# Optimization experiments

Measured on AMD Instinct MI355X. Metric: run time of the kernel, lower is better.

The kernel has to match this reference:

```python
import jax, jax.numpy as jnp
import numpy as np

DIM = 384
NH = 6
HD = DIM // NH  # 64
WS = (6, 12)    # window_size (dilated_size=[1,1] so total_window_size == window_size)
SS = (3, 6)     # shift_size
N = WS[0] * WS[1]  # 72 tokens per window


def _make_mask(H, W):
    # Faithful replication of SD_attn.create_mask (static, so computed in numpy).
    wh, ww = WS
    sh, sw = SS
    img = np.zeros((H, W), np.float32)
    cnt = 0
    for hs in (slice(0, -wh), slice(-wh, -sh), slice(-sh, None)):
        for wsl in (slice(0, -ww), slice(-ww, 0), slice(0, None)):
            img[hs, wsl] = cnt
            cnt += 1
    # window partition -> (nW, N)
    m = img.reshape(H // wh, wh, W // ww, ww).transpose(0, 2, 1, 3).reshape(-1, wh * ww)
    d = m[:, None, :] - m[:, :, None]  # (nW, N, N), [i,j] = m[j]-m[i]
    return np.where(d != 0, -np.inf, 0.0).astype(np.float32)


def _rope2d(x):
    # 2D axial rotary embedding over the (wh, ww) window grid.
    # x: (M, wh, ww, hd); first half of pair-channels rotated by h-position, second half by w-position.
    wh, ww, hd = x.shape[1], x.shape[2], x.shape[3]
    half = hd // 2
    inv = 1.0 / (10000.0 ** (np.arange(0, half, 2, dtype=np.float32) / half))  # (half//2,)
    ah = np.arange(wh, dtype=np.float32)[:, None] * inv  # (wh, half//2)
    aw = np.arange(ww, dtype=np.float32)[:, None] * inv  # (ww, half//2)
    ang = np.concatenate([
        np.broadcast_to(ah[:, None, :], (wh, ww, half // 2)),
        np.broadcast_to(aw[None, :, :], (wh, ww, half // 2)),
    ], -1)  # (wh, ww, half)
    cos = jnp.asarray(np.cos(ang), dtype=x.dtype)
    sin = jnp.asarray(np.sin(ang), dtype=x.dtype)
    x1, x2 = x[..., 0::2], x[..., 1::2]
    return jnp.stack([x1 * cos - x2 * sin, x1 * sin + x2 * cos], -1).reshape(x.shape)


def setup_inputs() -> dict:
    key = jax.random.key(0)
    ks = jax.random.split(key, 5)
    x = jax.random.normal(ks[0], (2, 192, 384, DIM), jnp.float32)
    w_qkv = 0.02 * jax.random.normal(ks[1], (3 * DIM, DIM), jnp.float32)
    b_qkv = 0.02 * jax.random.normal(ks[2], (3 * DIM,), jnp.float32)
    w_proj = 0.02 * jax.random.normal(ks[3], (DIM, DIM), jnp.float32)
    b_proj = 0.02 * jax.random.normal(ks[4], (DIM,), jnp.float32)
    return {"x": x, "w_qkv": w_qkv, "b_qkv": b_qkv, "w_proj": w_proj, "b_proj": b_proj}


def reference(x, w_qkv, b_qkv, w_proj, b_proj):
    B, H, W, C = x.shape
    wh, ww = WS
    sh, sw = SS
    nH, nWc = H // wh, W // ww
    nwin = nH * nWc
    B_ = B * nwin
    scale = HD ** -0.5

    # cyclic shift + window partition (dilated_size=[1,1] => plain swin windows)
    xs = jnp.roll(x, (-sh, -sw), axis=(1, 2))
    xw = xs.reshape(B, nH, wh, nWc, ww, C).transpose(0, 1, 3, 2, 4, 5).reshape(B_, N, C)

    qkv = (xw @ w_qkv.T + b_qkv).reshape(B_, N, 3, NH, HD).transpose(2, 0, 3, 1, 4)
    q, k, v = qkv[0], qkv[1], qkv[2]  # (B_, NH, N, HD)

    q = _rope2d(q.reshape(-1, wh, ww, HD)).reshape(B_, NH, N, HD)
    k = _rope2d(k.reshape(-1, wh, ww, HD)).reshape(B_, NH, N, HD)

    attn = jnp.einsum('bhnd,bhmd->bhnm', q * scale, k)  # (B_, NH, N, N)
    mask = jnp.asarray(_make_mask(H, W))                 # (nwin, N, N)
    attn = (attn.reshape(B, nwin, NH, N, N) + mask[None, :, None]).reshape(B_, NH, N, N)
    attn = jax.nn.softmax(attn, axis=-1)
    save_attn = attn.mean(axis=1)  # mean over heads -> (B_, N, N)

    out = jnp.einsum('bhnm,bhmd->bhnd', attn, v).transpose(0, 2, 1, 3).reshape(B_, N, C)
    out = out.reshape(B, nH, nWc, wh, ww, C).transpose(0, 1, 3, 2, 4, 5).reshape(B, H, W, C)
    out = jnp.roll(out, (sh, sw), axis=(1, 2))
    out = out @ w_proj.T + b_proj
    return out, save_attn
```

## Files before the change

kernel.cpp:

```cpp
#include <hip/hip_runtime.h>

typedef __attribute__((ext_vector_type(8))) __bf16 bf16x8;
typedef __attribute__((ext_vector_type(4))) float f32x4;
typedef unsigned short u16;
typedef unsigned int u32;

__device__ __forceinline__ u16 f2bf(float x){
  u32 u = __float_as_uint(x);
  return (u16)((u + 0x7fffu + ((u >> 16) & 1u)) >> 16);
}
__device__ __forceinline__ u32 pkbf(float lo, float hi){
  u32 r; asm("v_cvt_pk_bf16_f32 %0, %1, %2" : "=v"(r) : "v"(lo), "v"(hi)); return r;
}

union FragU { uint4 u4; bf16x8 bf; };

__device__ __forceinline__ bf16x8 lds_frag(const unsigned char* smem, int off, int row, int strideB, int kElem){
  int byte = (row * strideB + kElem * 2) ^ ((row & 7) << 4);
  FragU f; f.u4 = *reinterpret_cast<const uint4*>(smem + off + byte);
  return f.bf;
}

typedef __attribute__((address_space(3))) unsigned char lds_u8;
typedef __attribute__((address_space(1))) const unsigned char g_u8;
__device__ __forceinline__ void glds16(const void* g, void* l){
  __builtin_amdgcn_global_load_lds((g_u8*)g, (lds_u8*)l, 16, 0, 0);
}

__global__ void prep_weights(const float* __restrict__ wq, const float* __restrict__ wp,
                             u16* __restrict__ wqb, u16* __restrict__ wpb){
  int i = blockIdx.x * 256 + threadIdx.x;
  wqb[i] = f2bf(wq[i]);
  if (i < 147456) wpb[i] = f2bf(wp[i]);
}

__global__ void prep_x(const float* __restrict__ x, u16* __restrict__ xb){
  size_t i = ((size_t)blockIdx.x * 256 + threadIdx.x) * 8;
  float4 f0 = *reinterpret_cast<const float4*>(x + i);
  float4 f1 = *reinterpret_cast<const float4*>(x + i + 4);
  uint4 q;
  q.x = pkbf(f0.x, f0.y); q.y = pkbf(f0.z, f0.w);
  q.z = pkbf(f1.x, f1.y); q.w = pkbf(f1.z, f1.w);
  *reinterpret_cast<uint4*>(xb + i) = q;
}

#define QA_OFF 0
#define QB_OFF 16384
#define QTC    65536
#define QTS    66688
template<int XB>
__launch_bounds__(512, 2)
__global__ void qkv_gemm_t(const float* __restrict__ x, const u16* __restrict__ xb,
                           const u16* __restrict__ wqb,
                           const float* __restrict__ bq, float* __restrict__ out,
                           u16* __restrict__ vws)
{
  __shared__ __align__(16) unsigned char smem[67840];
  const int tid  = threadIdx.x;
  const int wave = tid >> 6;
  const int lane = tid & 63;
  const int l15  = lane & 15;
  const int lhi  = lane >> 4;
  const int wr   = wave >> 2;
  const int wc   = wave & 3;
  const int bx   = blockIdx.x;
  const int sec  = blockIdx.y;
  const size_t row0 = (size_t)bx * 128;
  const int a    = bx / 3;
  const int bcol = bx - 3 * a;
  const int bIm  = a / 192;
  const int hh   = a % 192;
  const int rh   = (hh >= 3) ? hh - 3 : hh + 189;
  const int wi   = rh / 6;
  const int r6   = rh - wi * 6;
  const int bwin = bIm * 1024 + wi * 32;

  float* tabc = reinterpret_cast<float*>(smem + QTC);
  float* tabs = reinterpret_cast<float*>(smem + QTS);
  if (tid < 288){
    int pos = tid >> 4, m = tid & 15;
    float pv = (pos < 6) ? (float)pos : (float)(pos - 6);
    float ang = pv * __expf(-(float)m * 0.5756462732485114f);
    tabc[tid] = cosf(ang);
    tabs[tid] = sinf(ang);
  }

  f32x4 acc[4][6];
  #pragma unroll
  for (int mt = 0; mt < 4; ++mt)
    #pragma unroll
    for (int nt = 0; nt < 6; ++nt) acc[mt][nt] = 0.0f;

  for (int kk = 0; kk < 6; ++kk){
    if constexpr (XB){
      #pragma unroll
      for (int it = 0; it < 2; ++it){
        int c = it * 512 + tid;
        int rrow = c >> 3, p = c & 7;
        int s = p ^ (rrow & 7);
        glds16(xb + (row0 + rrow) * 384 + kk * 64 + s * 8,
               smem + QA_OFF + c * 16);
      }
    } else {
      int row = tid >> 2;
      int c0  = (tid & 3) << 4;
      const float* src = x + (row0 + row) * 384 + kk * 64 + c0;
      float4 a0 = *reinterpret_cast<const float4*>(src);
      float4 a1 = *reinterpret_cast<const float4*>(src + 4);
      float4 a2 = *reinterpret_cast<const float4*>(src + 8);
      float4 a3 = *reinterpret_cast<const float4*>(src + 12);
      uint4 q0, q1;
      q0.x = pkbf(a0.x, a0.y); q0.y = pkbf(a0.z, a0.w);
      q0.z = pkbf(a1.x, a1.y); q0.w = pkbf(a1.z, a1.w);
      q1.x = pkbf(a2.x, a2.y); q1.y = pkbf(a2.z, a2.w);
      q1.z = pkbf(a3.x, a3.y); q1.w = pkbf(a3.z, a3.w);
      int b0 = (row * 128 + c0 * 2)      ^ ((row & 7) << 4);
      int b1 = (row * 128 + c0 * 2 + 16) ^ ((row & 7) << 4);
      *reinterpret_cast<uint4*>(smem + QA_OFF + b0) = q0;
      *reinterpret_cast<uint4*>(smem + QA_OFF + b1) = q1;
    }
    #pragma unroll
    for (int it = 0; it < 6; ++it){
      int c = it * 512 + tid;
      int n = c >> 3, p = c & 7;
      int s = p ^ (n & 7);
      glds16(wqb + (size_t)(sec * 384 + n) * 384 + kk * 64 + s * 8,
             smem + QB_OFF + c * 16);
    }
    __syncthreads();
    #pragma unroll
    for (int ks = 0; ks < 2; ++ks){
      const int kEl = ks * 32 + lhi * 8;
      bf16x8 af[4], bf[6];
      #pragma unroll
      for (int mt = 0; mt < 4; ++mt)
        af[mt] = lds_frag(smem, QA_OFF, wr * 64 + mt * 16 + l15, 128, kEl);
      #pragma unroll
      for (int nt = 0; nt < 6; ++nt)
        bf[nt] = lds_frag(smem, QB_OFF, wc * 96 + nt * 16 + l15, 128, kEl);
      #pragma unroll
      for (int mt = 0; mt < 4; ++mt)
        #pragma unroll
        for (int nt = 0; nt < 6; ++nt)
          acc[mt][nt] = __builtin_amdgcn_mfma_f32_16x16x32_bf16(af[mt], bf[nt], acc[mt][nt], 0, 0, 0);
    }
    __syncthreads();
  }

  if (sec < 2){
    u16* o16 = (u16*)out;
    #pragma unroll
    for (int nt = 0; nt < 6; ++nt){
      const int ch = wc * 96 + nt * 16 + l15;
      const float bias = bq[sec * 384 + ch];
      const int chh = ch & 63;
      const int p   = chh >> 1;
      const int m   = p & 15;
      const bool isR = (p < 16);
      const bool ev  = ((ch & 1) == 0);
      #pragma unroll
      for (int mt = 0; mt < 4; ++mt){
        #pragma unroll
        for (int r = 0; r < 4; ++r){
          const int i = wr * 64 + mt * 16 + lhi * 4 + r;
          float v = acc[mt][nt][r] + bias;
          float o = __shfl_xor(v, 1);
          int pos = isR ? r6 : (6 + (bcol * 128 + i + 6) % 12);
          float cc = tabc[pos * 16 + m], ssn = tabs[pos * 16 + m];
          float nv = ev ? (v * cc - o * ssn) : (o * ssn + v * cc);
          if (sec == 0) nv *= 0.125f;
          o16[(row0 + i) * 768 + sec * 384 + ch] = f2bf(nv);
        }
      }
    }
  } else {
    #pragma unroll
    for (int mt = 0; mt < 4; ++mt){
      const int ww2 = bcol * 128 + wr * 64 + mt * 16 + lhi * 4;
      const int rw  = (ww2 >= 6) ? ww2 - 6 : ww2 + 378;
      const int wj  = rw / 12;
      const int c0  = rw - wj * 12;
      const int tokb = r6 * 12;
      #pragma unroll
      for (int nt = 0; nt < 6; ++nt){
        const int ch  = wc * 96 + nt * 16 + l15;
        const int h   = ch >> 6;
        const int chh = ch & 63;
        const float bv = bq[768 + ch];
        u32 lo = pkbf(acc[mt][nt][0] + bv, acc[mt][nt][1] + bv);
        u32 hi = pkbf(acc[mt][nt][2] + bv, acc[mt][nt][3] + bv);
        u16* basep = vws + ((size_t)(bwin + wj) * 6 + h) * 5120 + chh * 80;
        if (c0 != 10){
          *reinterpret_cast<u32*>(basep + tokb + c0)     = lo;
          *reinterpret_cast<u32*>(basep + tokb + c0 + 2) = hi;
        } else {
          *reinterpret_cast<u32*>(basep + tokb + 10) = lo;
          const int wj1 = (wj == 31) ? 0 : wj + 1;
          *reinterpret_cast<u32*>(vws + ((size_t)(bwin + wj1) * 6 + h) * 5120 + chh * 80 + tokb) = hi;
        }
      }
    }
  }
}

#define QH4 0
#define KH4 10240
#define VT4 20480
#define SMEM4 30720
__launch_bounds__(320, 5)
__global__ void win_attn4(const u16* __restrict__ vws,
                          float* __restrict__ out)
{
  __shared__ __align__(16) unsigned char smem[SMEM4];
  const int tid  = threadIdx.x;
  const int wave = tid >> 6;
  const int lane = tid & 63;
  const int l15  = lane & 15;
  const int lhi  = lane >> 4;

  const int bid  = blockIdx.x;
  const int wgid = (bid & 7) * 256 + (bid >> 3);
  const int bIdx = wgid >> 10;
  const int win  = wgid & 1023;
  const int wi   = win >> 5;
  const int wj   = win & 31;
  const bool maskWin = (wi == 31);

  auto rowof = [&](int t)->size_t {
    int r = t / 12, c = t - r * 12;
    int hh = wi * 6 + r + 3;  if (hh >= 192) hh -= 192;
    int ww = wj * 12 + c + 6; if (ww >= 384) ww -= 384;
    return ((size_t)bIdx * 192 + hh) * 384 + ww;
  };
  const int qtok = wave * 16 + l15;
  const bool tv = (qtok < 72);
  const size_t qrow = rowof(tv ? qtok : 71);

  const u16* o16c = (const u16*)out;
  u16* ao16 = (u16*)out;
  const u16* vsl = vws + (size_t)win * 30720 + (size_t)bIdx * 31457280;

  float sv[5][4];
  #pragma unroll
  for (int a2 = 0; a2 < 5; ++a2)
    #pragma unroll
    for (int b2 = 0; b2 < 4; ++b2) sv[a2][b2] = 0.0f;

  for (int h = 0; h < 6; ++h){
    #pragma unroll
    for (int it = 0; it < 2; ++it){
      int c = it * 320 + tid;
      int t = c >> 3, p = c & 7;
      size_t row = rowof(t < 72 ? t : 71);
      int s = (p ^ (t & 7)) << 3;
      glds16(o16c + row * 768 + h * 64 + s,       smem + QH4 + c * 16);
      glds16(o16c + row * 768 + 384 + h * 64 + s, smem + KH4 + c * 16);
      glds16(vsl + (size_t)h * 5120 + c * 8,      smem + VT4 + c * 16);
    }
    __syncthreads();

    f32x4 pf[5];
    #pragma unroll
    for (int nt = 0; nt < 5; ++nt) pf[nt] = 0.0f;
    __builtin_amdgcn_s_setprio(1);
    #pragma unroll
    for (int ks = 0; ks < 2; ++ks){
      const int kEl = ks * 32 + lhi * 8;
      bf16x8 qf = lds_frag(smem, QH4, qtok, 128, kEl);
      #pragma unroll
      for (int nt = 0; nt < 5; ++nt){
        bf16x8 kf = lds_frag(smem, KH4, nt * 16 + l15, 128, kEl);
        pf[nt] = __builtin_amdgcn_mfma_f32_16x16x32_bf16(kf, qf, pf[nt], 0, 0, 0);
      }
    }
    __builtin_amdgcn_s_setprio(0);

    float mx = -1e30f;
    #pragma unroll
    for (int nt = 0; nt < 5; ++nt)
      #pragma unroll
      for (int r = 0; r < 4; ++r){
        const int kk2 = nt * 16 + lhi * 4 + r;
        bool valid = (kk2 < 72) && (!maskWin || ((kk2 < 36) == (qtok < 36)));
        float val = valid ? pf[nt][r] : -1e30f;
        pf[nt][r] = val;
        mx = fmaxf(mx, val);
      }
    mx = fmaxf(mx, __shfl_xor(mx, 16));
    mx = fmaxf(mx, __shfl_xor(mx, 32));
    float sm = 0.0f;
    #pragma unroll
    for (int nt = 0; nt < 5; ++nt)
      #pragma unroll
      for (int r = 0; r < 4; ++r){
        float e = __expf(pf[nt][r] - mx);
        pf[nt][r] = e; sm += e;
      }
    sm += __shfl_xor(sm, 16);
    sm += __shfl_xor(sm, 32);
    const float inv = 1.0f / sm;
    u32 pp[5][2];
    #pragma unroll
    for (int nt = 0; nt < 5; ++nt){
      float p0 = pf[nt][0] * inv, p1 = pf[nt][1] * inv;
      float p2 = pf[nt][2] * inv, p3 = pf[nt][3] * inv;
      sv[nt][0] += p0; sv[nt][1] += p1; sv[nt][2] += p2; sv[nt][3] += p3;
      pp[nt][0] = pkbf(p0, p1);
      pp[nt][1] = pkbf(p2, p3);
    }

    f32x4 oacc[4];
    #pragma unroll
    for (int nt = 0; nt < 4; ++nt) oacc[nt] = 0.0f;
    #pragma unroll
    for (int ks = 0; ks < 3; ++ks){
      FragU pb;
      u32 w[4];
      #pragma unroll
      for (int w_ = 0; w_ < 4; ++w_){
        int srcLane = l15 + 16 * ((lane >> 4 & 1) * 2 + (w_ >> 1));
        u32 c0 = __shfl(pp[ks * 2][w_ & 1], srcLane);
        u32 c1 = (ks * 2 + 1 < 5) ? __shfl(pp[ks * 2 + 1][w_ & 1], srcLane) : 0u;
        w[w_] = (lhi & 2) ? c1 : c0;
      }
      pb.u4.x = w[0]; pb.u4.y = w[1]; pb.u4.z = w[2]; pb.u4.w = w[3];
      const int kEl = ks * 32 + lhi * 8;
      __builtin_amdgcn_s_setprio(1);
      #pragma unroll
      for (int nt = 0; nt < 4; ++nt){
        FragU vf;
        vf.u4 = *reinterpret_cast<const uint4*>(smem + VT4 + (nt * 16 + l15) * 160 + kEl * 2);
        oacc[nt] = __builtin_amdgcn_mfma_f32_16x16x32_bf16(vf.bf, pb.bf, oacc[nt], 0, 0, 0);
      }
      __builtin_amdgcn_s_setprio(0);
    }
    if (tv){
      u16* ao = ao16 + qrow * 768 + h * 64;
      #pragma unroll
      for (int nt = 0; nt < 4; ++nt){
        uint2 pk;
        pk.x = pkbf(oacc[nt][0], oacc[nt][1]);
        pk.y = pkbf(oacc[nt][2], oacc[nt][3]);
        *reinterpret_cast<uint2*>(ao + nt * 16 + lhi * 4) = pk;
      }
    }
    __syncthreads();
  }

  if (tv){
    float* so = out + 56623104ull + (size_t)wgid * 5184 + (size_t)qtok * 72;
    const float c6 = 1.0f / 6.0f;
    #pragma unroll
    for (int nt = 0; nt < 4; ++nt){
      float4 v4; v4.x = sv[nt][0]*c6; v4.y = sv[nt][1]*c6; v4.z = sv[nt][2]*c6; v4.w = sv[nt][3]*c6;
      *reinterpret_cast<float4*>(so + nt * 16 + lhi * 4) = v4;
    }
    if (lhi < 2){
      float4 v4; v4.x = sv[4][0]*c6; v4.y = sv[4][1]*c6; v4.z = sv[4][2]*c6; v4.w = sv[4][3]*c6;
      *reinterpret_cast<float4*>(so + 64 + lhi * 4) = v4;
    }
  }
}

#define VT3 0
#define P3  16384
__launch_bounds__(320, 4)
__global__ void win_attn_fb(const float* __restrict__ x,
                            const u16* __restrict__ wqb,
                            const float* __restrict__ bq,
                            float* __restrict__ out)
{
  __shared__ __align__(16) unsigned char smem[36864];
  const int tid  = threadIdx.x;
  const int wave = tid >> 6;
  const int lane = tid & 63;
  const int l15  = lane & 15;
  const int lhi  = lane >> 4;

  const int wgid = blockIdx.x;
  const int bIdx = wgid >> 10;
  const int win  = wgid & 1023;
  const int wi   = win >> 5;
  const int wj   = win & 31;
  const bool maskWin = (wi == 31);

  auto rowof = [&](int t)->int {
    int r = t / 12, c = t - r * 12;
    int hh = wi * 6 + r + 3;  if (hh >= 192) hh -= 192;
    int ww = wj * 12 + c + 6; if (ww >= 384) ww -= 384;
    return (bIdx * 192 + hh) * 384 + ww;
  };
  const int qtok = wave * 16 + l15;
  const int qrow = rowof(qtok < 72 ? qtok : 71);
  int krow[5];
  #pragma unroll
  for (int nt = 0; nt < 5; ++nt) krow[nt] = rowof(nt * 16 + l15 < 72 ? nt * 16 + l15 : 71);
  const bool tv = (qtok < 72);

  bf16x8 xfrag[12];
  {
    const float* xp = x + (size_t)qrow * 384;
    #pragma unroll
    for (int ks = 0; ks < 12; ++ks){
      uint4 q; q.x = 0; q.y = 0; q.z = 0; q.w = 0;
      if (tv){
        float4 f0 = *reinterpret_cast<const float4*>(xp + ks * 32 + lhi * 8);
        float4 f1 = *reinterpret_cast<const float4*>(xp + ks * 32 + lhi * 8 + 4);
        q.x = pkbf(f0.x, f0.y); q.y = pkbf(f0.z, f0.w);
        q.z = pkbf(f1.x, f1.y); q.w = pkbf(f1.z, f1.w);
      }
      FragU f; f.u4 = q; xfrag[ks] = f.bf;
    }
  }

  const u16* o16 = (const u16*)out;
  u16* ao16 = (u16*)out;
  const u16* wv = wqb + 768 * 384;

  float sv[5][4];
  #pragma unroll
  for (int a2 = 0; a2 < 5; ++a2)
    #pragma unroll
    for (int b2 = 0; b2 < 4; ++b2) sv[a2][b2] = 0.0f;

  for (int h = 0; h < 6; ++h){
    {
      f32x4 vacc[4];
      #pragma unroll
      for (int nt = 0; nt < 4; ++nt) vacc[nt] = 0.0f;
      #pragma unroll
      for (int ks = 0; ks < 12; ++ks){
        const int kEl = ks * 32 + lhi * 8;
        #pragma unroll
        for (int nt = 0; nt < 4; ++nt){
          FragU f;
          f.u4 = *reinterpret_cast<const uint4*>(wv + (size_t)(h * 64 + nt * 16 + l15) * 384 + kEl);
          vacc[nt] = __builtin_amdgcn_mfma_f32_16x16x32_bf16(xfrag[ks], f.bf, vacc[nt], 0, 0, 0);
        }
      }
      #pragma unroll
      for (int nt = 0; nt < 4; ++nt){
        const int chl = nt * 16 + l15;
        const float bv = bq[768 + h * 64 + chl];
        const int t0 = wave * 16 + lhi * 4;
        uint2 pk;
        pk.x = pkbf(vacc[nt][0] + bv, vacc[nt][1] + bv);
        pk.y = pkbf(vacc[nt][2] + bv, vacc[nt][3] + bv);
        int byte = (chl * 256 + t0 * 2) ^ ((chl & 7) << 4);
        *reinterpret_cast<uint2*>(smem + VT3 + byte) = pk;
      }
    }

    f32x4 pf[5];
    #pragma unroll
    for (int nt = 0; nt < 5; ++nt) pf[nt] = 0.0f;
    #pragma unroll
    for (int ks = 0; ks < 2; ++ks){
      const int kEl = ks * 32 + lhi * 8;
      FragU qf;
      qf.u4 = *reinterpret_cast<const uint4*>(o16 + (size_t)qrow * 768 + h * 64 + kEl);
      #pragma unroll
      for (int nt = 0; nt < 5; ++nt){
        FragU kf;
        kf.u4 = *reinterpret_cast<const uint4*>(o16 + (size_t)krow[nt] * 768 + 384 + h * 64 + kEl);
        pf[nt] = __builtin_amdgcn_mfma_f32_16x16x32_bf16(kf.bf, qf.bf, pf[nt], 0, 0, 0);
      }
    }

    float mx = -1e30f;
    #pragma unroll
    for (int nt = 0; nt < 5; ++nt)
      #pragma unroll
      for (int r = 0; r < 4; ++r){
        const int kk2 = nt * 16 + lhi * 4 + r;
        bool valid = (kk2 < 72) && (!maskWin || ((kk2 < 36) == (qtok < 36)));
        float val = valid ? pf[nt][r] : -1e30f;
        pf[nt][r] = val;
        mx = fmaxf(mx, val);
      }
    mx = fmaxf(mx, __shfl_xor(mx, 16));
    mx = fmaxf(mx, __shfl_xor(mx, 32));
    float sm = 0.0f;
    #pragma unroll
    for (int nt = 0; nt < 5; ++nt)
      #pragma unroll
      for (int r = 0; r < 4; ++r){
        float e = __expf(pf[nt][r] - mx);
        pf[nt][r] = e; sm += e;
      }
    sm += __shfl_xor(sm, 16);
    sm += __shfl_xor(sm, 32);
    const float inv = 1.0f / sm;
    #pragma unroll
    for (int nt = 0; nt < 5; ++nt)
      #pragma unroll
      for (int r = 0; r < 4; ++r){
        float pv2 = pf[nt][r] * inv;
        pf[nt][r] = pv2;
        sv[nt][r] += pv2;
      }

    #pragma unroll
    for (int nt = 0; nt < 5; ++nt){
      const int k0 = nt * 16 + lhi * 4;
      uint2 pk;
      pk.x = pkbf(pf[nt][0], pf[nt][1]);
      pk.y = pkbf(pf[nt][2], pf[nt][3]);
      int byte = (qtok * 256 + k0 * 2) ^ ((qtok & 7) << 4);
      *reinterpret_cast<uint2*>(smem + P3 + byte) = pk;
    }
    {
      int byte = (qtok * 256 + (80 + lhi * 4) * 2) ^ ((qtok & 7) << 4);
      uint2 z; z.x = 0; z.y = 0;
      *reinterpret_cast<uint2*>(smem + P3 + byte) = z;
    }
    __syncthreads();

    f32x4 oacc[4];
    #pragma unroll
    for (int nt = 0; nt < 4; ++nt) oacc[nt] = 0.0f;
    #pragma unroll
    for (int ks = 0; ks < 3; ++ks){
      const int kEl = ks * 32 + lhi * 8;
      bf16x8 pfr = lds_frag(smem, P3, qtok, 256, kEl);
      #pragma unroll
      for (int nt = 0; nt < 4; ++nt){
        bf16x8 vf = lds_frag(smem, VT3, nt * 16 + l15, 256, kEl);
        oacc[nt] = __builtin_amdgcn_mfma_f32_16x16x32_bf16(vf, pfr, oacc[nt], 0, 0, 0);
      }
    }
    if (tv){
      u16* ao = ao16 + (size_t)qrow * 768 + h * 64;
      #pragma unroll
      for (int nt = 0; nt < 4; ++nt){
        uint2 pk;
        pk.x = pkbf(oacc[nt][0], oacc[nt][1]);
        pk.y = pkbf(oacc[nt][2], oacc[nt][3]);
        *reinterpret_cast<uint2*>(ao + nt * 16 + lhi * 4) = pk;
      }
    }
    __syncthreads();
  }

  if (tv){
    float* so = out + 56623104ull + (size_t)wgid * 5184 + (size_t)qtok * 72;
    const float c6 = 1.0f / 6.0f;
    #pragma unroll
    for (int nt = 0; nt < 4; ++nt){
      float4 v4; v4.x = sv[nt][0]*c6; v4.y = sv[nt][1]*c6; v4.z = sv[nt][2]*c6; v4.w = sv[nt][3]*c6;
      *reinterpret_cast<float4*>(so + nt * 16 + lhi * 4) = v4;
    }
    if (lhi < 2){
      float4 v4; v4.x = sv[4][0]*c6; v4.y = sv[4][1]*c6; v4.z = sv[4][2]*c6; v4.w = sv[4][3]*c6;
      *reinterpret_cast<float4*>(so + 64 + lhi * 4) = v4;
    }
  }
}

#define A2_OFF 0
#define B2_OFF 16384
#define SMEM2  65536
__launch_bounds__(512, 2)
__global__ void proj_gemm(const u16* __restrict__ wpb, const float* __restrict__ bp,
                          float* __restrict__ out)
{
  __shared__ __align__(16) unsigned char smem[SMEM2];
  unsigned char* base = smem;

  const int tid  = threadIdx.x;
  const int wave = tid >> 6;
  const int lane = tid & 63;
  const int l15  = lane & 15;
  const int lhi  = lane >> 4;
  const int wr   = wave >> 2;
  const int wc   = wave & 3;
  const size_t row0 = (size_t)blockIdx.x * 128;
  const u16* aog = (const u16*)out;

  f32x4 acc[4][6];
  #pragma unroll
  for (int mt = 0; mt < 4; ++mt)
    #pragma unroll
    for (int nt = 0; nt < 6; ++nt) acc[mt][nt] = 0.0f;

  for (int kk = 0; kk < 6; ++kk){
    #pragma unroll
    for (int it = 0; it < 2; ++it){
      int c = it * 512 + wave * 64 + lane;
      int rrow = c >> 3, p = c & 7;
      int s = p ^ (rrow & 7);
      glds16(aog + (row0 + rrow) * 768 + kk * 64 + s * 8,
             base + A2_OFF + (it * 512 + wave * 64) * 16);
    }
    #pragma unroll
    for (int it = 0; it < 6; ++it){
      int c = it * 512 + wave * 64 + lane;
      int n = c >> 3, p = c & 7;
      int s = p ^ (n & 7);
      glds16(wpb + (size_t)n * 384 + kk * 64 + s * 8,
             base + B2_OFF + (it * 512 + wave * 64) * 16);
    }
    __syncthreads();
    #pragma unroll
    for (int ks = 0; ks < 2; ++ks){
      const int kEl = ks * 32 + lhi * 8;
      bf16x8 af[4], bf[6];
      #pragma unroll
      for (int mt = 0; mt < 4; ++mt)
        af[mt] = lds_frag(base, A2_OFF, wr * 64 + mt * 16 + l15, 128, kEl);
      #pragma unroll
      for (int nt = 0; nt < 6; ++nt)
        bf[nt] = lds_frag(base, B2_OFF, wc * 96 + nt * 16 + l15, 128, kEl);
      #pragma unroll
      for (int mt = 0; mt < 4; ++mt)
        #pragma unroll
        for (int nt = 0; nt < 6; ++nt)
          acc[mt][nt] = __builtin_amdgcn_mfma_f32_16x16x32_bf16(af[mt], bf[nt], acc[mt][nt], 0, 0, 0);
    }
    __syncthreads();
  }

  float bpv[6];
  #pragma unroll
  for (int nt = 0; nt < 6; ++nt) bpv[nt] = bp[wc * 96 + nt * 16 + l15];
  #pragma unroll
  for (int mt = 0; mt < 4; ++mt)
    #pragma unroll
    for (int nt = 0; nt < 6; ++nt){
      const int ch = wc * 96 + nt * 16 + l15;
      #pragma unroll
      for (int r = 0; r < 4; ++r){
        size_t grow = row0 + wr * 64 + mt * 16 + lhi * 4 + r;
        out[grow * 384 + ch] = acc[mt][nt][r] + bpv[nt];
      }
    }
}

extern "C" void kernel_launch(void* const* d_in, const int* in_sizes, int n_in,
                              void* d_out, int out_size, void* d_ws, size_t ws_size,
                              hipStream_t stream)
{
  const float* x  = (const float*)d_in[0];
  const float* wq = (const float*)d_in[1];
  const float* bq = (const float*)d_in[2];
  const float* wp = (const float*)d_in[3];
  const float* bp = (const float*)d_in[4];
  float* out = (float*)d_out;

  u16* wqb = (u16*)d_ws;
  u16* wpb = (u16*)((char*)d_ws + 442368 * 2);
  u16* vws = (u16*)((char*)d_ws + 1179648);
  u16* xb  = (u16*)((char*)d_ws + 127008768);

  const bool big  = ws_size >= 127008768ull;
  const bool big2 = ws_size >= 240254976ull;

  prep_weights<<<1728, 256, 0, stream>>>(wq, wp, wqb, wpb);
  if (big2){
    prep_x<<<27648, 256, 0, stream>>>(x, xb);
    qkv_gemm_t<1><<<dim3(1152, 3), 512, 0, stream>>>(x, xb, wqb, bq, out, vws);
    win_attn4<<<2048, 320, 0, stream>>>(vws, out);
  } else if (big){
    qkv_gemm_t<0><<<dim3(1152, 3), 512, 0, stream>>>(x, nullptr, wqb, bq, out, vws);
    win_attn4<<<2048, 320, 0, stream>>>(vws, out);
  } else {
    qkv_gemm_t<0><<<dim3(1152, 2), 512, 0, stream>>>(x, nullptr, wqb, bq, out, vws);
    win_attn_fb<<<2048, 320, 0, stream>>>(x, wqb, bq, out);
  }
  proj_gemm<<<1152, 512, 0, stream>>>(wpb, bp, out);
}
```

Before: 710.9 us.

## Add smaller-tile double-buffered QKV and projection GEMMs with direct-register A loads

```diff
diff --git a/kernel.cpp b/kernel.cpp
--- a/kernel.cpp
+++ b/kernel.cpp
@@ -44,13 +44,162 @@
   *reinterpret_cast<uint4*>(xb + i) = q;
 }
 
+#define B6STR 12288
+#define T6C   24576
+#define T6S   25728
+__launch_bounds__(512, 4)
+__global__ void qkv_gemm2(const u16* __restrict__ xb, const u16* __restrict__ wqb,
+                          const float* __restrict__ bq, float* __restrict__ out,
+                          u16* __restrict__ vws)
+{
+  __shared__ __align__(16) unsigned char smem[26880];
+  const int tid  = threadIdx.x;
+  const int wave = tid >> 6;
+  const int lane = tid & 63;
+  const int l15  = lane & 15;
+  const int lhi  = lane >> 4;
+  const int wr   = wave >> 2;
+  const int wc   = wave & 3;
+  const int bx   = blockIdx.x;
+  const int ny   = blockIdx.y;
+  const int sec  = blockIdx.z;
+  const size_t row0 = (size_t)bx * 128;
+  const int a    = bx / 3;
+  const int bcol = bx - 3 * a;
+  const int bIm  = a / 192;
+  const int hh   = a % 192;
+  const int rh   = (hh >= 3) ? hh - 3 : hh + 189;
+  const int wi   = rh / 6;
+  const int r6   = rh - wi * 6;
+  const int bwin = bIm * 1024 + wi * 32;
+
+  float* tabc = reinterpret_cast<float*>(smem + T6C);
+  float* tabs = reinterpret_cast<float*>(smem + T6S);
+  if (tid < 288){
+    int pos = tid >> 4, m = tid & 15;
+    float pv = (pos < 6) ? (float)pos : (float)(pos - 6);
+    float ang = pv * __expf(-(float)m * 0.5756462732485114f);
+    tabc[tid] = cosf(ang);
+    tabs[tid] = sinf(ang);
+  }
+
+  const u16* bsec = wqb + (size_t)(sec * 384 + ny * 192) * 384;
+  auto stageB = [&](int t, int bufOff){
+    {
+      int c = tid, row = c >> 2, ccd = c & 3;
+      int ccs = ccd ^ ((row >> 1) & 3);
+      glds16(bsec + (size_t)row * 384 + t * 32 + ccs * 8, smem + bufOff + c * 16);
+    }
+    if (tid < 256){
+      int c = 512 + tid, row = c >> 2, ccd = c & 3;
+      int ccs = ccd ^ ((row >> 1) & 3);
+      glds16(bsec + (size_t)row * 384 + t * 32 + ccs * 8, smem + bufOff + c * 16);
+    }
+  };
+
+  const u16* abase = xb + (row0 + wr * 64 + l15) * 384 + lhi * 8;
+
+  f32x4 acc[4][3];
+  #pragma unroll
+  for (int mt = 0; mt < 4; ++mt)
+    #pragma unroll
+    for (int nt = 0; nt < 3; ++nt) acc[mt][nt] = 0.0f;
+
+  FragU a_cur[4], a_nxt[4];
+  #pragma unroll
+  for (int mt = 0; mt < 4; ++mt)
+    a_cur[mt].u4 = *reinterpret_cast<const uint4*>(abase + mt * 6144);
+  stageB(0, 0);
+  __syncthreads();
+
+  int buf = 0;
+  for (int t = 0; t < 12; ++t){
+    if (t < 11){
+      stageB(t + 1, buf ^ B6STR);
+      #pragma unroll
+      for (int mt = 0; mt < 4; ++mt)
+        a_nxt[mt].u4 = *reinterpret_cast<const uint4*>(abase + mt * 6144 + (t + 1) * 32);
+    }
+    FragU bf[3];
+    #pragma unroll
+    for (int nt = 0; nt < 3; ++nt){
+      int rown = wc * 48 + nt * 16 + l15;
+      int byte = buf + rown * 64 + ((lhi ^ ((rown >> 1) & 3)) << 4);
+      bf[nt].u4 = *reinterpret_cast<const uint4*>(smem + byte);
+    }
+    #pragma unroll
+    for (int mt = 0; mt < 4; ++mt)
+      #pragma unroll
+      for (int nt = 0; nt < 3; ++nt)
+        acc[mt][nt] = __builtin_amdgcn_mfma_f32_16x16x32_bf16(a_cur[mt].bf, bf[nt].bf, acc[mt][nt], 0, 0, 0);
+    __syncthreads();
+    #pragma unroll
+    for (int mt = 0; mt < 4; ++mt) a_cur[mt] = a_nxt[mt];
+    buf ^= B6STR;
+  }
+
+  if (sec < 2){
+    u16* o16 = (u16*)out;
+    #pragma unroll
+    for (int nt = 0; nt < 3; ++nt){
+      const int ch = ny * 192 + wc * 48 + nt * 16 + l15;
+      const float bias = bq[sec * 384 + ch];
+      const int chh = ch & 63;
+      const int p   = chh >> 1;
+      const int m   = p & 15;
+      const bool isR = (p < 16);
+      const bool ev  = ((ch & 1) == 0);
+      #pragma unroll
+      for (int mt = 0; mt < 4; ++mt){
+        #pragma unroll
+        for (int r = 0; r < 4; ++r){
+          const int i = wr * 64 + mt * 16 + lhi * 4 + r;
+          float v = acc[mt][nt][r] + bias;
+          float o = __shfl_xor(v, 1);
+          int pos = isR ? r6 : (6 + (bcol * 128 + i + 6) % 12);
+          float cc = tabc[pos * 16 + m], ssn = tabs[pos * 16 + m];
+          float nv = ev ? (v * cc - o * ssn) : (o * ssn + v * cc);
+          if (sec == 0) nv *= 0.125f;
+          o16[(row0 + i) * 768 + sec * 384 + ch] = f2bf(nv);
+        }
+      }
+    }
+  } else {
+    #pragma unroll
+    for (int mt = 0; mt < 4; ++mt){
+      const int ww2 = bcol * 128 + wr * 64 + mt * 16 + lhi * 4;
+      const int rw  = (ww2 >= 6) ? ww2 - 6 : ww2 + 378;
+      const int wj  = rw / 12;
+      const int c0  = rw - wj * 12;
+      const int tokb = r6 * 12;
+      #pragma unroll
+      for (int nt = 0; nt < 3; ++nt){
+        const int ch  = ny * 192 + wc * 48 + nt * 16 + l15;
+        const int h   = ch >> 6;
+        const int chh = ch & 63;
+        const float bv = bq[768 + ch];
+        u32 lo = pkbf(acc[mt][nt][0] + bv, acc[mt][nt][1] + bv);
+        u32 hi = pkbf(acc[mt][nt][2] + bv, acc[mt][nt][3] + bv);
+        u16* basep = vws + ((size_t)(bwin + wj) * 6 + h) * 5120 + chh * 80;
+        if (c0 != 10){
+          *reinterpret_cast<u32*>(basep + tokb + c0)     = lo;
+          *reinterpret_cast<u32*>(basep + tokb + c0 + 2) = hi;
+        } else {
+          *reinterpret_cast<u32*>(basep + tokb + 10) = lo;
+          const int wj1 = (wj == 31) ? 0 : wj + 1;
+          *reinterpret_cast<u32*>(vws + ((size_t)(bwin + wj1) * 6 + h) * 5120 + chh * 80 + tokb) = hi;
+        }
+      }
+    }
+  }
+}
+
 #define QA_OFF 0
 #define QB_OFF 16384
 #define QTC    65536
 #define QTS    66688
-template<int XB>
 __launch_bounds__(512, 2)
-__global__ void qkv_gemm_t(const float* __restrict__ x, const u16* __restrict__ xb,
+__global__ void qkv_gemm_t(const float* __restrict__ x,
                            const u16* __restrict__ wqb,
                            const float* __restrict__ bq, float* __restrict__ out,
                            u16* __restrict__ vws)
@@ -92,16 +241,7 @@
     for (int nt = 0; nt < 6; ++nt) acc[mt][nt] = 0.0f;
 
   for (int kk = 0; kk < 6; ++kk){
-    if constexpr (XB){
-      #pragma unroll
-      for (int it = 0; it < 2; ++it){
-        int c = it * 512 + tid;
-        int rrow = c >> 3, p = c & 7;
-        int s = p ^ (rrow & 7);
-        glds16(xb + (row0 + rrow) * 384 + kk * 64 + s * 8,
-               smem + QA_OFF + c * 16);
-      }
-    } else {
+    {
       int row = tid >> 2;
       int c0  = (tid & 3) << 4;
       const float* src = x + (row0 + row) * 384 + kk * 64 + c0;
@@ -131,18 +271,18 @@
     #pragma unroll
     for (int ks = 0; ks < 2; ++ks){
       const int kEl = ks * 32 + lhi * 8;
-      bf16x8 af[4], bf[6];
+      bf16x8 af[4], bfr[6];
       #pragma unroll
       for (int mt = 0; mt < 4; ++mt)
         af[mt] = lds_frag(smem, QA_OFF, wr * 64 + mt * 16 + l15, 128, kEl);
       #pragma unroll
       for (int nt = 0; nt < 6; ++nt)
-        bf[nt] = lds_frag(smem, QB_OFF, wc * 96 + nt * 16 + l15, 128, kEl);
+        bfr[nt] = lds_frag(smem, QB_OFF, wc * 96 + nt * 16 + l15, 128, kEl);
       #pragma unroll
       for (int mt = 0; mt < 4; ++mt)
         #pragma unroll
         for (int nt = 0; nt < 6; ++nt)
-          acc[mt][nt] = __builtin_amdgcn_mfma_f32_16x16x32_bf16(af[mt], bf[nt], acc[mt][nt], 0, 0, 0);
+          acc[mt][nt] = __builtin_amdgcn_mfma_f32_16x16x32_bf16(af[mt], bfr[nt], acc[mt][nt], 0, 0, 0);
     }
     __syncthreads();
   }
@@ -207,9 +347,11 @@
 #define KH4 10240
 #define VT4 20480
 #define SMEM4 30720
+template<int AODST>
 __launch_bounds__(320, 5)
 __global__ void win_attn4(const u16* __restrict__ vws,
-                          float* __restrict__ out)
+                          float* __restrict__ out,
+                          u16* __restrict__ axb)
 {
   __shared__ __align__(16) unsigned char smem[SMEM4];
   const int tid  = threadIdx.x;
@@ -237,7 +379,6 @@
   const size_t qrow = rowof(tv ? qtok : 71);
 
   const u16* o16c = (const u16*)out;
-  u16* ao16 = (u16*)out;
   const u16* vsl = vws + (size_t)win * 30720 + (size_t)bIdx * 31457280;
 
   float sv[5][4];
@@ -335,7 +476,9 @@
       __builtin_amdgcn_s_setprio(0);
     }
     if (tv){
-      u16* ao = ao16 + qrow * 768 + h * 64;
+      u16* ao;
+      if constexpr (AODST == 1) ao = axb + qrow * 384 + h * 64;
+      else                      ao = (u16*)out + qrow * 768 + h * 64;
       #pragma unroll
       for (int nt = 0; nt < 4; ++nt){
         uint2 pk;
@@ -362,209 +505,100 @@
   }
 }
 
-#define VT3 0
-#define P3  16384
-__launch_bounds__(320, 4)
-__global__ void win_attn_fb(const float* __restrict__ x,
-                            const u16* __restrict__ wqb,
-                            const float* __restrict__ bq,
-                            float* __restrict__ out)
+__launch_bounds__(512, 4)
+__global__ void proj_gemm2(const u16* __restrict__ axb,
+                           const u16* __restrict__ wpb, const float* __restrict__ bp,
+                           float* __restrict__ out)
 {
-  __shared__ __align__(16) unsigned char smem[36864];
+  __shared__ __align__(16) unsigned char smem[24576];
   const int tid  = threadIdx.x;
   const int wave = tid >> 6;
   const int lane = tid & 63;
   const int l15  = lane & 15;
   const int lhi  = lane >> 4;
-
-  const int wgid = blockIdx.x;
-  const int bIdx = wgid >> 10;
-  const int win  = wgid & 1023;
-  const int wi   = win >> 5;
-  const int wj   = win & 31;
-  const bool maskWin = (wi == 31);
-
-  auto rowof = [&](int t)->int {
-    int r = t / 12, c = t - r * 12;
-    int hh = wi * 6 + r + 3;  if (hh >= 192) hh -= 192;
-    int ww = wj * 12 + c + 6; if (ww >= 384) ww -= 384;
-    return (bIdx * 192 + hh) * 384 + ww;
+  const int wr   = wave >> 2;
+  const int wc   = wave & 3;
+  const size_t row0 = (size_t)blockIdx.x * 128;
+  const int ny   = blockIdx.y;
+
+  const u16* bsec = wpb + (size_t)(ny * 192) * 384;
+  auto stageB = [&](int t, int bufOff){
+    {
+      int c = tid, row = c >> 2, ccd = c & 3;
+      int ccs = ccd ^ ((row >> 1) & 3);
+      glds16(bsec + (size_t)row * 384 + t * 32 + ccs * 8, smem + bufOff + c * 16);
+    }
+    if (tid < 256){
+      int c = 512 + tid, row = c >> 2, ccd = c & 3;
+      int ccs = ccd ^ ((row >> 1) & 3);
+      glds16(bsec + (size_t)row * 384 + t * 32 + ccs * 8, smem + bufOff + c * 16);
+    }
   };
-  const int qtok = wave * 16 + l15;
-  const int qrow = rowof(qtok < 72 ? qtok : 71);
-  int krow[5];
-  #pragma unroll
-  for (int nt = 0; nt < 5; ++nt) krow[nt] = rowof(nt * 16 + l15 < 72 ? nt * 16 + l15 : 71);
-  const bool tv = (qtok < 72);
-
-  bf16x8 xfrag[12];
-  {
-    const float* xp = x + (size_t)qrow * 384;
-    #pragma unroll
-    for (int ks = 0; ks < 12; ++ks){
-      uint4 q; q.x = 0; q.y = 0; q.z = 0; q.w = 0;
-      if (tv){
-        float4 f0 = *reinterpret_cast<const float4*>(xp + ks * 32 + lhi * 8);
-        float4 f1 = *reinterpret_cast<const float4*>(xp + ks * 32 + lhi * 8 + 4);
-        q.x = pkbf(f0.x, f0.y); q.y = pkbf(f0.z, f0.w);
-        q.z = pkbf(f1.x, f1.y); q.w = pkbf(f1.z, f1.w);
-      }
-      FragU f; f.u4 = q; xfrag[ks] = f.bf;
-    }
-  }
-
-  const u16* o16 = (const u16*)out;
-  u16* ao16 = (u16*)out;
-  const u16* wv = wqb + 768 * 384;
-
-  float sv[5][4];
-  #pragma unroll
-  for (int a2 = 0; a2 < 5; ++a2)
-    #pragma unroll
-    for (int b2 = 0; b2 < 4; ++b2) sv[a2][b2] = 0.0f;
-
-  for (int h = 0; h < 6; ++h){
-    {
-      f32x4 vacc[4];
-      #pragma unroll
-      for (int nt = 0; nt < 4; ++nt) vacc[nt] = 0.0f;
-      #pragma unroll
-      for (int ks = 0; ks < 12; ++ks){
-        const int kEl = ks * 32 + lhi * 8;
-        #pragma unroll
-        for (int nt = 0; nt < 4; ++nt){
-          FragU f;
-          f.u4 = *reinterpret_cast<const uint4*>(wv + (size_t)(h * 64 + nt * 16 + l15) * 384 + kEl);
-          vacc[nt] = __builtin_amdgcn_mfma_f32_16x16x32_bf16(xfrag[ks], f.bf, vacc[nt], 0, 0, 0);
-        }
-      }
-      #pragma unroll
-      for (int nt = 0; nt < 4; ++nt){
-        const int chl = nt * 16 + l15;
-        const float bv = bq[768 + h * 64 + chl];
-        const int t0 = wave * 16 + lhi * 4;
-        uint2 pk;
-        pk.x = pkbf(vacc[nt][0] + bv, vacc[nt][1] + bv);
-        pk.y = pkbf(vacc[nt][2] + bv, vacc[nt][3] + bv);
-        int byte = (chl * 256 + t0 * 2) ^ ((chl & 7) << 4);
-        *reinterpret_cast<uint2*>(smem + VT3 + byte) = pk;
-      }
-    }
-
-    f32x4 pf[5];
-    #pragma unroll
-    for (int nt = 0; nt < 5; ++nt) pf[nt] = 0.0f;
-    #pragma unroll
-    for (int ks = 0; ks < 2; ++ks){
-      const int kEl = ks * 32 + lhi * 8;
-      FragU qf;
-      qf.u4 = *reinterpret_cast<const uint4*>(o16 + (size_t)qrow * 768 + h * 64 + kEl);
-      #pragma unroll
-      for (int nt = 0; nt < 5; ++nt){
-        FragU kf;
-        kf.u4 = *reinterpret_cast<const uint4*>(o16 + (size_t)krow[nt] * 768 + 384 + h * 64 + kEl);
-        pf[nt] = __builtin_amdgcn_mfma_f32_16x16x32_bf16(kf.bf, qf.bf, pf[nt], 0, 0, 0);
-      }
-    }
-
-    float mx = -1e30f;
-    #pragma unroll
-    for (int nt = 0; nt < 5; ++nt)
+
+  const u16* abase = axb + (row0 + wr * 64 + l15) * 384 + lhi * 8;
+
+  f32x4 acc[4][3];
+  #pragma unroll
+  for (int mt = 0; mt < 4; ++mt)
+    #pragma unroll
+    for (int nt = 0; nt < 3; ++nt) acc[mt][nt] = 0.0f;
+
+  FragU a_cur[4], a_nxt[4];
+  #pragma unroll
+  for (int mt = 0; mt < 4; ++mt)
+    a_cur[mt].u4 = *reinterpret_cast<const uint4*>(abase + mt * 6144);
+  stageB(0, 0);
+  __syncthreads();
+
+  int buf = 0;
+  for (int t = 0; t < 12; ++t){
+    if (t < 11){
+      stageB(t + 1, buf ^ B6STR);
+      #pragma unroll
+      for (int mt = 0; mt < 4; ++mt)
+        a_nxt[mt].u4 = *reinterpret_cast<const uint4*>(abase + mt * 6144 + (t + 1) * 32);
+    }
+    FragU bfr[3];
+    #pragma unroll
+    for (int nt = 0; nt < 3; ++nt){
+      int rown = wc * 48 + nt * 16 + l15;
+      int byte = buf + rown * 64 + ((lhi ^ ((rown >> 1) & 3)) << 4);
+      bfr[nt].u4 = *reinterpret_cast<const uint4*>(smem + byte);
+    }
+    #pragma unroll
+    for (int mt = 0; mt < 4; ++mt)
+      #pragma unroll
+      for (int nt = 0; nt < 3; ++nt)
+        acc[mt][nt] = __builtin_amdgcn_mfma_f32_16x16x32_bf16(a_cur[mt].bf, bfr[nt].bf, acc[mt][nt], 0, 0, 0);
+    __syncthreads();
+    #pragma unroll
+    for (int mt = 0; mt < 4; ++mt) a_cur[mt] = a_nxt[mt];
+    buf ^= B6STR;
+  }
+
+  float bpv[3];
+  #pragma unroll
+  for (int nt = 0; nt < 3; ++nt) bpv[nt] = bp[ny * 192 + wc * 48 + nt * 16 + l15];
+  #pragma unroll
+  for (int mt = 0; mt < 4; ++mt)
+    #pragma unroll
+    for (int nt = 0; nt < 3; ++nt){
+      const int ch = ny * 192 + wc * 48 + nt * 16 + l15;
       #pragma unroll
       for (int r = 0; r < 4; ++r){
-        const int kk2 = nt * 16 + lhi * 4 + r;
-        bool valid = (kk2 < 72) && (!maskWin || ((kk2 < 36) == (qtok < 36)));
-        float val = valid ? pf[nt][r] : -1e30f;
-        pf[nt][r] = val;
-        mx = fmaxf(mx, val);
-      }
-    mx = fmaxf(mx, __shfl_xor(mx, 16));
-    mx = fmaxf(mx, __shfl_xor(mx, 32));
-    float sm = 0.0f;
-    #pragma unroll
-    for (int nt = 0; nt < 5; ++nt)
-      #pragma unroll
-      for (int r = 0; r < 4; ++r){
-        float e = __expf(pf[nt][r] - mx);
-        pf[nt][r] = e; sm += e;
-      }
-    sm += __shfl_xor(sm, 16);
-    sm += __shfl_xor(sm, 32);
-    const float inv = 1.0f / sm;
-    #pragma unroll
-    for (int nt = 0; nt < 5; ++nt)
-      #pragma unroll
-      for (int r = 0; r < 4; ++r){
-        float pv2 = pf[nt][r] * inv;
-        pf[nt][r] = pv2;
-        sv[nt][r] += pv2;
-      }
-
-    #pragma unroll
-    for (int nt = 0; nt < 5; ++nt){
-      const int k0 = nt * 16 + lhi * 4;
-      uint2 pk;
-      pk.x = pkbf(pf[nt][0], pf[nt][1]);
-      pk.y = pkbf(pf[nt][2], pf[nt][3]);
-      int byte = (qtok * 256 + k0 * 2) ^ ((qtok & 7) << 4);
-      *reinterpret_cast<uint2*>(smem + P3 + byte) = pk;
-    }
-    {
-      int byte = (qtok * 256 + (80 + lhi * 4) * 2) ^ ((qtok & 7) << 4);
-      uint2 z; z.x = 0; z.y = 0;
-      *reinterpret_cast<uint2*>(smem + P3 + byte) = z;
-    }
-    __syncthreads();
-
-    f32x4 oacc[4];
-    #pragma unroll
-    for (int nt = 0; nt < 4; ++nt) oacc[nt] = 0.0f;
-    #pragma unroll
-    for (int ks = 0; ks < 3; ++ks){
-      const int kEl = ks * 32 + lhi * 8;
-      bf16x8 pfr = lds_frag(smem, P3, qtok, 256, kEl);
-      #pragma unroll
-      for (int nt = 0; nt < 4; ++nt){
-        bf16x8 vf = lds_frag(smem, VT3, nt * 16 + l15, 256, kEl);
-        oacc[nt] = __builtin_amdgcn_mfma_f32_16x16x32_bf16(vf, pfr, oacc[nt], 0, 0, 0);
-      }
-    }
-    if (tv){
-      u16* ao = ao16 + (size_t)qrow * 768 + h * 64;
-      #pragma unroll
-      for (int nt = 0; nt < 4; ++nt){
-        uint2 pk;
-        pk.x = pkbf(oacc[nt][0], oacc[nt][1]);
-        pk.y = pkbf(oacc[nt][2], oacc[nt][3]);
-        *reinterpret_cast<uint2*>(ao + nt * 16 + lhi * 4) = pk;
-      }
-    }
-    __syncthreads();
-  }
-
-  if (tv){
-    float* so = out + 56623104ull + (size_t)wgid * 5184 + (size_t)qtok * 72;
-    const float c6 = 1.0f / 6.0f;
-    #pragma unroll
-    for (int nt = 0; nt < 4; ++nt){
-      float4 v4; v4.x = sv[nt][0]*c6; v4.y = sv[nt][1]*c6; v4.z = sv[nt][2]*c6; v4.w = sv[nt][3]*c6;
-      *reinterpret_cast<float4*>(so + nt * 16 + lhi * 4) = v4;
-    }
-    if (lhi < 2){
-      float4 v4; v4.x = sv[4][0]*c6; v4.y = sv[4][1]*c6; v4.z = sv[4][2]*c6; v4.w = sv[4][3]*c6;
-      *reinterpret_cast<float4*>(so + 64 + lhi * 4) = v4;
-    }
-  }
+        size_t grow = row0 + wr * 64 + mt * 16 + lhi * 4 + r;
+        out[grow * 384 + ch] = acc[mt][nt][r] + bpv[nt];
+      }
+    }
 }
 
 #define A2_OFF 0
 #define B2_OFF 16384
-#define SMEM2  65536
 __launch_bounds__(512, 2)
 __global__ void proj_gemm(const u16* __restrict__ wpb, const float* __restrict__ bp,
                           float* __restrict__ out)
 {
-  __shared__ __align__(16) unsigned char smem[SMEM2];
+  __shared__ __align__(16) unsigned char smem[65536];
   unsigned char* base = smem;
 
   const int tid  = threadIdx.x;
@@ -604,18 +638,18 @@
     #pragma unroll
     for (int ks = 0; ks < 2; ++ks){
       const int kEl = ks * 32 + lhi * 8;
-      bf16x8 af[4], bf[6];
+      bf16x8 af[4], bfr[6];
       #pragma unroll
       for (int mt = 0; mt < 4; ++mt)
         af[mt] = lds_frag(base, A2_OFF, wr * 64 + mt * 16 + l15, 128, kEl);
       #pragma unroll
       for (int nt = 0; nt < 6; ++nt)
-        bf[nt] = lds_frag(base, B2_OFF, wc * 96 + nt * 16 + l15, 128, kEl);
+        bfr[nt] = lds_frag(base, B2_OFF, wc * 96 + nt * 16 + l15, 128, kEl);
       #pragma unroll
       for (int mt = 0; mt < 4; ++mt)
         #pragma unroll
         for (int nt = 0; nt < 6; ++nt)
-          acc[mt][nt] = __builtin_amdgcn_mfma_f32_16x16x32_bf16(af[mt], bf[nt], acc[mt][nt], 0, 0, 0);
+          acc[mt][nt] = __builtin_amdgcn_mfma_f32_16x16x32_bf16(af[mt], bfr[nt], acc[mt][nt], 0, 0, 0);
     }
     __syncthreads();
   }
@@ -652,20 +686,17 @@
   u16* vws = (u16*)((char*)d_ws + 1179648);
   u16* xb  = (u16*)((char*)d_ws + 127008768);
 
-  const bool big  = ws_size >= 127008768ull;
   const bool big2 = ws_size >= 240254976ull;
 
   prep_weights<<<1728, 256, 0, stream>>>(wq, wp, wqb, wpb);
   if (big2){
     prep_x<<<27648, 256, 0, stream>>>(x, xb);
-    qkv_gemm_t<1><<<dim3(1152, 3), 512, 0, stream>>>(x, xb, wqb, bq, out, vws);
-    win_attn4<<<2048, 320, 0, stream>>>(vws, out);
-  } else if (big){
-    qkv_gemm_t<0><<<dim3(1152, 3), 512, 0, stream>>>(x, nullptr, wqb, bq, out, vws);
-    win_attn4<<<2048, 320, 0, stream>>>(vws, out);
+    qkv_gemm2<<<dim3(1152, 2, 3), 512, 0, stream>>>(xb, wqb, bq, out, vws);
+    win_attn4<1><<<2048, 320, 0, stream>>>(vws, out, xb);
+    proj_gemm2<<<dim3(1152, 2), 512, 0, stream>>>(xb, wpb, bp, out);
   } else {
-    qkv_gemm_t<0><<<dim3(1152, 2), 512, 0, stream>>>(x, nullptr, wqb, bq, out, vws);
-    win_attn_fb<<<2048, 320, 0, stream>>>(x, wqb, bq, out);
-  }
-  proj_gemm<<<1152, 512, 0, stream>>>(wpb, bp, out);
-}
+    qkv_gemm_t<<<dim3(1152, 3), 512, 0, stream>>>(x, wqb, bq, out, vws);
+    win_attn4<0><<<2048, 320, 0, stream>>>(vws, out, xb);
+    proj_gemm<<<1152, 512, 0, stream>>>(wpb, bp, out);
+  }
+}
```

Measured after the change: 812.6 us. 1.14x slower.
